# Performance work log

Measured on AMD Instinct MI355X. Metric: run time of the kernel, lower is better.

The kernel has to match this reference:

```python
import jax, jax.numpy as jnp
import numpy as np

D = 256; DFFN = 1024; H = 8; NLVL = 4; NPNT = 4; HD = D // H
BS = 4; NQ = 100; NPTS = 25
SPATIAL = [(128, 128), (64, 64), (32, 32), (16, 16)]
LEN_IN = sum(h * w for h, w in SPATIAL)


def _ln(x, g, b, eps=1e-5):
    m = x.mean(-1, keepdims=True)
    v = ((x - m) ** 2).mean(-1, keepdims=True)
    return (x - m) * jax.lax.rsqrt(v + eps) * g + b


def _mha(q, k, v, w_in, b_in, w_out, b_out):
    # torch nn.MultiheadAttention math, batch-first layout [B,S,D]
    B, Sq, _ = q.shape; Sk = k.shape[1]
    wq, wk, wv = jnp.split(w_in, 3, 0); bq, bk, bv = jnp.split(b_in, 3)
    qh = (q @ wq.T + bq).reshape(B, Sq, H, HD).transpose(0, 2, 1, 3)
    kh = (k @ wk.T + bk).reshape(B, Sk, H, HD).transpose(0, 2, 1, 3)
    vh = (v @ wv.T + bv).reshape(B, Sk, H, HD).transpose(0, 2, 1, 3)
    a = jax.nn.softmax(jnp.einsum('bhqd,bhkd->bhqk', qh, kh) * (1.0 / float(np.sqrt(HD))), -1)
    o = jnp.einsum('bhqk,bhkd->bhqd', a, vh).transpose(0, 2, 1, 3).reshape(B, Sq, D)
    return o @ w_out.T + b_out


def _msdeform(query, ref, src, off_w, off_b, aw_w, aw_b, val_w, val_b, out_w, out_b):
    # MSDeformAttn: per-query multi-level bilinear sampling + weighted aggregation
    bs, Lq, _ = query.shape
    value = (src @ val_w.T + val_b).reshape(bs, LEN_IN, H, HD)
    off = (query @ off_w.T + off_b).reshape(bs, Lq, H, NLVL, NPNT, 2)
    aw = jax.nn.softmax((query @ aw_w.T + aw_b).reshape(bs, Lq, H, NLVL * NPNT), -1)
    aw = aw.reshape(bs, Lq, H, NLVL, NPNT)
    norm = jnp.array([[w, h] for h, w in SPATIAL], jnp.float32)  # (W,H) per level
    loc = ref[:, :, None, :, None, :] + off / norm[None, None, None, :, None, :]
    out = jnp.zeros((bs, H, Lq, HD), query.dtype)
    start = 0
    for l, (hh, ww) in enumerate(SPATIAL):
        v_l = value[:, start:start + hh * ww].transpose(0, 2, 1, 3)  # [bs,H,hw,HD]
        start += hh * ww
        # grid_sample align_corners=False pixel coords: loc*size - 0.5
        x = (loc[:, :, :, l, :, 0] * ww - 0.5).transpose(0, 2, 1, 3).reshape(bs, H, Lq * NPNT)
        y = (loc[:, :, :, l, :, 1] * hh - 0.5).transpose(0, 2, 1, 3).reshape(bs, H, Lq * NPNT)
        x0 = jnp.floor(x); y0 = jnp.floor(y); wx = x - x0; wy = y - y0
        x0i = x0.astype(jnp.int32); y0i = y0.astype(jnp.int32); x1i = x0i + 1; y1i = y0i + 1
        def g(xi, yi):
            valid = ((xi >= 0) & (xi < ww) & (yi >= 0) & (yi < hh)).astype(query.dtype)
            idx = jnp.clip(yi, 0, hh - 1) * ww + jnp.clip(xi, 0, ww - 1)
            return jnp.take_along_axis(v_l, idx[..., None], axis=2) * valid[..., None]
        s = (g(x0i, y0i) * ((1 - wx) * (1 - wy))[..., None]
             + g(x1i, y0i) * (wx * (1 - wy))[..., None]
             + g(x0i, y1i) * ((1 - wx) * wy)[..., None]
             + g(x1i, y1i) * (wx * wy)[..., None])
        s = s.reshape(bs, H, Lq, NPNT, HD)
        out = out + (s * aw[:, :, :, l].transpose(0, 2, 1, 3)[..., None]).sum(3)
    return out.transpose(0, 2, 1, 3).reshape(bs, Lq, D) @ out_w.T + out_b


def _fwd(tgt, query_pos, reference_points, src,
         w_in_intra, b_in_intra, w_out_intra, b_out_intra, g_norm_intra, b_norm_intra,
         w_in_inter, b_in_inter, w_out_inter, b_out_inter, g_norm_inter, b_norm_inter,
         off_w, off_b, aw_w, aw_b, val_w, val_b, co_w, co_b, g_norm_cross, b_norm_cross,
         lin1_w, lin1_b, lin2_w, lin2_b, g_norm3, b_norm3):
    bs, nq, npts, d = tgt.shape
    # intra-instance self-attention (over control points)
    q = (tgt + query_pos).reshape(bs * nq, npts, d)
    t2 = _mha(q, q, tgt.reshape(bs * nq, npts, d), w_in_intra, b_in_intra, w_out_intra, b_out_intra)
    tgt = _ln(tgt + t2.reshape(bs, nq, npts, d), g_norm_intra, b_norm_intra)
    # inter-instance self-attention (over queries), no pos embed per source code
    ti = tgt.transpose(0, 2, 1, 3).reshape(bs * npts, nq, d)
    t2 = _mha(ti, ti, ti, w_in_inter, b_in_inter, w_out_inter, b_out_inter)
    ti = _ln(ti + t2, g_norm_inter, b_norm_inter).reshape(bs, npts, nq, d).transpose(0, 2, 1, 3)
    # deformable cross-attention
    ref = jnp.broadcast_to(reference_points[:, :, None], (bs, nq, npts, NLVL, 2)).reshape(bs, nq * npts, NLVL, 2)
    qc = (ti + query_pos).reshape(bs, nq * npts, d)
    t2 = _msdeform(qc, ref, src, off_w, off_b, aw_w, aw_b, val_w, val_b, co_w, co_b).reshape(bs, nq, npts, d)
    tgt = _ln(ti + t2, g_norm_cross, b_norm_cross)
    # FFN
    ff = jax.nn.relu(tgt @ lin1_w.T + lin1_b) @ lin2_w.T + lin2_b
    return _ln(tgt + ff, g_norm3, b_norm3)


def setup_inputs() -> dict:
    key = jax.random.key(0)
    ki = iter(jax.random.split(key, 40))
    def rn(shape, sc=0.02):
        return jax.random.normal(next(ki), shape, jnp.float32) * sc
    inp = dict(
        tgt=jax.random.normal(next(ki), (BS, NQ, NPTS, D), jnp.float32),
        query_pos=jax.random.normal(next(ki), (BS, NQ, NPTS, D), jnp.float32),
        reference_points=jax.random.uniform(next(ki), (BS, NQ, NLVL, 2), jnp.float32),
        src=jax.random.normal(next(ki), (BS, LEN_IN, D), jnp.float32),
        w_in_intra=rn((3 * D, D)), b_in_intra=jnp.zeros((3 * D,), jnp.float32),
        w_out_intra=rn((D, D)), b_out_intra=jnp.zeros((D,), jnp.float32),
        g_norm_intra=jnp.ones((D,), jnp.float32), b_norm_intra=jnp.zeros((D,), jnp.float32),
        w_in_inter=rn((3 * D, D)), b_in_inter=jnp.zeros((3 * D,), jnp.float32),
        w_out_inter=rn((D, D)), b_out_inter=jnp.zeros((D,), jnp.float32),
        g_norm_inter=jnp.ones((D,), jnp.float32), b_norm_inter=jnp.zeros((D,), jnp.float32),
        off_w=rn((H * NLVL * NPNT * 2, D), 0.001), off_b=rn((H * NLVL * NPNT * 2,), 0.5),
        aw_w=rn((H * NLVL * NPNT, D)), aw_b=jnp.zeros((H * NLVL * NPNT,), jnp.float32),
        val_w=rn((D, D)), val_b=jnp.zeros((D,), jnp.float32),
        co_w=rn((D, D)), co_b=jnp.zeros((D,), jnp.float32),
        g_norm_cross=jnp.ones((D,), jnp.float32), b_norm_cross=jnp.zeros((D,), jnp.float32),
        lin1_w=rn((DFFN, D)), lin1_b=jnp.zeros((DFFN,), jnp.float32),
        lin2_w=rn((D, DFFN)), lin2_b=jnp.zeros((D,), jnp.float32),
        g_norm3=jnp.ones((D,), jnp.float32), b_norm3=jnp.zeros((D,), jnp.float32),
        src_spatial_shapes=jnp.array(SPATIAL, jnp.int32),
        level_start_index=jnp.array(np.cumsum([0] + [h * w for h, w in SPATIAL[:-1]]), jnp.int32),
    )
    return inp


def reference(tgt, query_pos, reference_points, src,
              w_in_intra, b_in_intra, w_out_intra, b_out_intra, g_norm_intra, b_norm_intra,
              w_in_inter, b_in_inter, w_out_inter, b_out_inter, g_norm_inter, b_norm_inter,
              off_w, off_b, aw_w, aw_b, val_w, val_b, co_w, co_b, g_norm_cross, b_norm_cross,
              lin1_w, lin1_b, lin2_w, lin2_b, g_norm3, b_norm3,
              src_spatial_shapes, level_start_index):
    # spatial shapes / level starts are compile-time constants (SPATIAL); args kept for signature parity
    return _fwd(tgt, query_pos, reference_points, src,
                w_in_intra, b_in_intra, w_out_intra, b_out_intra, g_norm_intra, b_norm_intra,
                w_in_inter, b_in_inter, w_out_inter, b_out_inter, g_norm_inter, b_norm_inter,
                off_w, off_b, aw_w, aw_b, val_w, val_b, co_w, co_b, g_norm_cross, b_norm_cross,
                lin1_w, lin1_b, lin2_w, lin2_b, g_norm3, b_norm3)
```

## Files before the change

### kernel.cpp

```cpp
#include <hip/hip_runtime.h>
#include <math.h>

#define DMODEL 256
#define HEADS  8
#define HDIM   32
#define BS     4
#define NQ     100
#define NPTS   25
#define LQ     2500
#define M10K   10000
#define LEN_IN 21760
#define MVAL   87040

typedef float f32x4 __attribute__((ext_vector_type(4)));
typedef short s16x8 __attribute__((ext_vector_type(8)));
typedef unsigned short u16;

static __device__ __forceinline__ short f2bf(float f) {
    unsigned u = __builtin_bit_cast(unsigned, f);
    u = (u + 0x7fffu + ((u >> 16) & 1u)) >> 16;
    return (short)u;
}
static __device__ __forceinline__ unsigned pack2(float lo, float hi) {
    return (unsigned)(u16)f2bf(lo) | ((unsigned)(u16)f2bf(hi) << 16);
}
static __device__ __forceinline__ float bf_lo(unsigned u) {
    return __builtin_bit_cast(float, u << 16);
}
static __device__ __forceinline__ float bf_hi(unsigned u) {
    return __builtin_bit_cast(float, u & 0xffff0000u);
}

#define LDSK   40
#define LDSK64 72

__global__ __launch_bounds__(256) void convert_weights_kernel(
    const float* __restrict__ s0, const float* __restrict__ s1,
    const float* __restrict__ s2, const float* __restrict__ s3,
    const float* __restrict__ s4, const float* __restrict__ s5,
    const float* __restrict__ s6, const float* __restrict__ s7,
    const float* __restrict__ s8, const float* __restrict__ s9,
    u16* __restrict__ dst)
{
    int t8 = (blockIdx.x * 256 + threadIdx.x) * 8;
    if (t8 >= 1277952) return;
    const float* s; int base;
    if      (t8 <  196608) { s = s0; base = 0;       }
    else if (t8 <  262144) { s = s1; base = 196608;  }
    else if (t8 <  458752) { s = s2; base = 262144;  }
    else if (t8 <  524288) { s = s3; base = 458752;  }
    else if (t8 <  589824) { s = s4; base = 524288;  }
    else if (t8 <  622592) { s = s5; base = 589824;  }
    else if (t8 <  688128) { s = s6; base = 622592;  }
    else if (t8 <  753664) { s = s7; base = 688128;  }
    else if (t8 < 1015808) { s = s8; base = 753664;  }
    else                   { s = s9; base = 1015808; }
    const float* p = s + (t8 - base);
    float4 a = *(const float4*)p;
    float4 b = *(const float4*)(p + 4);
    s16x8 v;
    v[0]=f2bf(a.x); v[1]=f2bf(a.y); v[2]=f2bf(a.z); v[3]=f2bf(a.w);
    v[4]=f2bf(b.x); v[5]=f2bf(b.y); v[6]=f2bf(b.z); v[7]=f2bf(b.w);
    *(s16x8*)(dst + t8) = v;
}

__global__ __launch_bounds__(256) void add_convert_kernel(
    const float* __restrict__ a, const float* __restrict__ b,
    u16* __restrict__ xb, u16* __restrict__ ab, int n8)
{
    int i = blockIdx.x * 256 + threadIdx.x;
    if (i >= n8) return;
    size_t o = (size_t)i * 8;
    float4 a0 = *(const float4*)(a + o);
    float4 a1 = *(const float4*)(a + o + 4);
    if (ab) {
        s16x8 v;
        v[0]=f2bf(a0.x); v[1]=f2bf(a0.y); v[2]=f2bf(a0.z); v[3]=f2bf(a0.w);
        v[4]=f2bf(a1.x); v[5]=f2bf(a1.y); v[6]=f2bf(a1.z); v[7]=f2bf(a1.w);
        *(s16x8*)(ab + o) = v;
    }
    if (b) {
        float4 b0 = *(const float4*)(b + o);
        float4 b1 = *(const float4*)(b + o + 4);
        a0.x += b0.x; a0.y += b0.y; a0.z += b0.z; a0.w += b0.w;
        a1.x += b1.x; a1.y += b1.y; a1.z += b1.z; a1.w += b1.w;
    }
    s16x8 v;
    v[0]=f2bf(a0.x); v[1]=f2bf(a0.y); v[2]=f2bf(a0.z); v[3]=f2bf(a0.w);
    v[4]=f2bf(a1.x); v[5]=f2bf(a1.y); v[6]=f2bf(a1.z); v[7]=f2bf(a1.w);
    *(s16x8*)(xb + o) = v;
}

__global__ __launch_bounds__(256) void gemm_mfma_kernel(
    const u16* __restrict__ A, int lda,
    const u16* __restrict__ W, int K,
    const float* __restrict__ bias,
    void* __restrict__ Cv, int ldc,
    int M, int relu, int out_bf16)
{
    __shared__ short As[64 * LDSK64];
    __shared__ short Ws[64 * LDSK64];

    const int tid = threadIdx.x;
    const int m0 = blockIdx.y * 64, n0 = blockIdx.x * 64;
    const int srow = tid >> 2;
    const int sk = (tid & 3) * 16;
    const int wave = tid >> 6;
    const int wm = wave & 1, wn = wave >> 1;
    const int lane = tid & 63;
    const int lrow = lane & 15;
    const int kq = lane >> 4;

    const int gm = m0 + srow;
    const u16* aptr = A + (size_t)gm * lda + sk;
    const u16* wptr = W + (size_t)(n0 + srow) * K + sk;

    f32x4 acc[2][2];
#pragma unroll
    for (int i = 0; i < 2; ++i)
#pragma unroll
        for (int j = 0; j < 2; ++j) acc[i][j] = (f32x4)(0.f);

    s16x8 a0 = (s16x8)0, a1 = (s16x8)0, w0, w1;
    if (gm < M) { a0 = *(const s16x8*)aptr; a1 = *(const s16x8*)(aptr + 8); }
    w0 = *(const s16x8*)wptr; w1 = *(const s16x8*)(wptr + 8);

    for (int k0 = 0; k0 < K; k0 += 64) {
        *(s16x8*)&As[srow * LDSK64 + sk]     = a0;
        *(s16x8*)&As[srow * LDSK64 + sk + 8] = a1;
        *(s16x8*)&Ws[srow * LDSK64 + sk]     = w0;
        *(s16x8*)&Ws[srow * LDSK64 + sk + 8] = w1;
        __syncthreads();
        if (k0 + 64 < K) {
            if (gm < M) {
                a0 = *(const s16x8*)(aptr + k0 + 64);
                a1 = *(const s16x8*)(aptr + k0 + 72);
            }
            w0 = *(const s16x8*)(wptr + k0 + 64);
            w1 = *(const s16x8*)(wptr + k0 + 72);
        }

#pragma unroll
        for (int s = 0; s < 2; ++s) {
            s16x8 af[2], bfv[2];
#pragma unroll
            for (int i = 0; i < 2; ++i)
                af[i] = *(const s16x8*)&As[(wm * 32 + i * 16 + lrow) * LDSK64 + s * 32 + kq * 8];
#pragma unroll
            for (int j = 0; j < 2; ++j)
                bfv[j] = *(const s16x8*)&Ws[(wn * 32 + j * 16 + lrow) * LDSK64 + s * 32 + kq * 8];
#pragma unroll
            for (int i = 0; i < 2; ++i)
#pragma unroll
                for (int j = 0; j < 2; ++j)
                    acc[i][j] = __builtin_amdgcn_mfma_f32_16x16x32_bf16(af[i], bfv[j], acc[i][j], 0, 0, 0);
        }
        __syncthreads();
    }

#pragma unroll
    for (int i = 0; i < 2; ++i)
#pragma unroll
        for (int j = 0; j < 2; ++j) {
            int col = n0 + wn * 32 + j * 16 + lrow;
            float bv = bias[col];
#pragma unroll
            for (int reg = 0; reg < 4; ++reg) {
                int gmo = m0 + wm * 32 + i * 16 + kq * 4 + reg;
                if (gmo < M) {
                    float v = acc[i][j][reg] + bv;
                    if (relu) v = fmaxf(v, 0.f);
                    if (out_bf16)
                        ((u16*)Cv)[(size_t)gmo * ldc + col] = (u16)f2bf(v);
                    else
                        ((float*)Cv)[(size_t)gmo * ldc + col] = v;
                }
            }
        }
}

__global__ __launch_bounds__(256) void gemm_mfma128_kernel(
    const u16* __restrict__ A, int lda,
    const u16* __restrict__ W, int K,
    const float* __restrict__ bias,
    void* __restrict__ Cv, int ldc,
    int M, int relu, int out_bf16)
{
    __shared__ short As[128 * LDSK];
    __shared__ short Ws[128 * LDSK];

    const int tid = threadIdx.x;
    const int m0 = blockIdx.y * 128, n0 = blockIdx.x * 128;

    const int srow = tid >> 1;
    const int sk = (tid & 1) * 16;

    const int wave = tid >> 6;
    const int wm = wave & 1, wn = wave >> 1;
    const int lane = tid & 63;
    const int lrow = lane & 15;
    const int kq = lane >> 4;

    const int gm = m0 + srow;
    const u16* aptr = A + (size_t)gm * lda + sk;
    const u16* wptr = W + (size_t)(n0 + srow) * K + sk;

    f32x4 acc[4][4];
#pragma unroll
    for (int i = 0; i < 4; ++i)
#pragma unroll
        for (int j = 0; j < 4; ++j) acc[i][j] = (f32x4)(0.f);

    s16x8 a0 = (s16x8)0, a1 = (s16x8)0, w0, w1;
    if (gm < M) { a0 = *(const s16x8*)aptr; a1 = *(const s16x8*)(aptr + 8); }
    w0 = *(const s16x8*)wptr; w1 = *(const s16x8*)(wptr + 8);

    for (int k0 = 0; k0 < K; k0 += 32) {
        *(s16x8*)&As[srow * LDSK + sk]     = a0;
        *(s16x8*)&As[srow * LDSK + sk + 8] = a1;
        *(s16x8*)&Ws[srow * LDSK + sk]     = w0;
        *(s16x8*)&Ws[srow * LDSK + sk + 8] = w1;
        __syncthreads();
        if (k0 + 32 < K) {
            if (gm < M) {
                a0 = *(const s16x8*)(aptr + k0 + 32);
                a1 = *(const s16x8*)(aptr + k0 + 40);
            }
            w0 = *(const s16x8*)(wptr + k0 + 32);
            w1 = *(const s16x8*)(wptr + k0 + 40);
        }

        s16x8 af[4], bfv[4];
#pragma unroll
        for (int i = 0; i < 4; ++i)
            af[i] = *(const s16x8*)&As[(wm * 64 + i * 16 + lrow) * LDSK + kq * 8];
#pragma unroll
        for (int j = 0; j < 4; ++j)
            bfv[j] = *(const s16x8*)&Ws[(wn * 64 + j * 16 + lrow) * LDSK + kq * 8];
#pragma unroll
        for (int i = 0; i < 4; ++i)
#pragma unroll
            for (int j = 0; j < 4; ++j)
                acc[i][j] = __builtin_amdgcn_mfma_f32_16x16x32_bf16(af[i], bfv[j], acc[i][j], 0, 0, 0);
        __syncthreads();
    }

#pragma unroll
    for (int i = 0; i < 4; ++i)
#pragma unroll
        for (int j = 0; j < 4; ++j) {
            int col = n0 + wn * 64 + j * 16 + lrow;
            float bv = bias[col];
#pragma unroll
            for (int reg = 0; reg < 4; ++reg) {
                int gmo = m0 + wm * 64 + i * 16 + kq * 4 + reg;
                if (gmo < M) {
                    float v = acc[i][j][reg] + bv;
                    if (relu) v = fmaxf(v, 0.f);
                    if (out_bf16)
                        ((u16*)Cv)[(size_t)gmo * ldc + col] = (u16)f2bf(v);
                    else
                        ((float*)Cv)[(size_t)gmo * ldc + col] = v;
                }
            }
        }
}

__global__ __launch_bounds__(256) void gemm_value64_kernel(
    const float* __restrict__ A,
    const u16* __restrict__ W,
    const float* __restrict__ bias,
    u16* __restrict__ C)
{
    __shared__ short As[64 * LDSK];
    __shared__ short Ws[128 * LDSK];

    const int tid = threadIdx.x;
    const int n0 = blockIdx.x * 128;
    const int m0 = blockIdx.y * 64;

    const int arow = tid >> 2;
    const int ak = (tid & 3) * 8;
    const int wrow = tid >> 1;
    const int wk = (tid & 1) * 16;

    const float* aptr = A + (size_t)(m0 + arow) * 256 + ak;
    const u16* wptr = W + (size_t)(n0 + wrow) * 256 + wk;

    const int wave = tid >> 6;
    const int wm = wave & 1, wn = wave >> 1;
    const int lane = tid & 63;
    const int lrow = lane & 15, kq = lane >> 4;

    f32x4 acc[2][4];
#pragma unroll
    for (int i = 0; i < 2; ++i)
#pragma unroll
        for (int j = 0; j < 4; ++j) acc[i][j] = (f32x4)(0.f);

    float4 pa0 = *(const float4*)aptr;
    float4 pa1 = *(const float4*)(aptr + 4);
    s16x8 w0 = *(const s16x8*)wptr;
    s16x8 w1 = *(const s16x8*)(wptr + 8);

    for (int k0 = 0; k0 < 256; k0 += 32) {
        s16x8 av;
        av[0]=f2bf(pa0.x); av[1]=f2bf(pa0.y); av[2]=f2bf(pa0.z); av[3]=f2bf(pa0.w);
        av[4]=f2bf(pa1.x); av[5]=f2bf(pa1.y); av[6]=f2bf(pa1.z); av[7]=f2bf(pa1.w);
        *(s16x8*)&As[arow * LDSK + ak]     = av;
        *(s16x8*)&Ws[wrow * LDSK + wk]     = w0;
        *(s16x8*)&Ws[wrow * LDSK + wk + 8] = w1;
        __syncthreads();
        if (k0 + 32 < 256) {
            pa0 = *(const float4*)(aptr + k0 + 32);
            pa1 = *(const float4*)(aptr + k0 + 36);
            w0 = *(const s16x8*)(wptr + k0 + 32);
            w1 = *(const s16x8*)(wptr + k0 + 40);
        }

        s16x8 af[2], bfv[4];
#pragma unroll
        for (int i = 0; i < 2; ++i)
            af[i] = *(const s16x8*)&As[(wm * 32 + i * 16 + lrow) * LDSK + kq * 8];
#pragma unroll
        for (int j = 0; j < 4; ++j)
            bfv[j] = *(const s16x8*)&Ws[(wn * 64 + j * 16 + lrow) * LDSK + kq * 8];
#pragma unroll
        for (int i = 0; i < 2; ++i)
#pragma unroll
            for (int j = 0; j < 4; ++j)
                acc[i][j] = __builtin_amdgcn_mfma_f32_16x16x32_bf16(af[i], bfv[j], acc[i][j], 0, 0, 0);
        __syncthreads();
    }

#pragma unroll
    for (int i = 0; i < 2; ++i)
#pragma unroll
        for (int j = 0; j < 4; ++j) {
            int col = n0 + wn * 64 + j * 16 + lrow;
            float bv = bias[col];
#pragma unroll
            for (int reg = 0; reg < 4; ++reg) {
                int gmo = m0 + wm * 32 + i * 16 + kq * 4 + reg;
                C[(size_t)gmo * 256 + col] = (u16)f2bf(acc[i][j][reg] + bv);
            }
        }
}

__global__ __launch_bounds__(256) void inter_attn_mfma_kernel(
    const u16* __restrict__ qkv, u16* __restrict__ out, float scale)
{
    __shared__ __align__(16) u16 Qs[112 * 40];
    __shared__ __align__(16) u16 Ks[112 * 40];
    __shared__ __align__(16) u16 Vt[32 * 136];
    __shared__ __align__(16) u16 Ps[112 * 136];

    const int b = blockIdx.x, h = blockIdx.y;
    const u16* base = qkv + (size_t)b * 100 * 768;
    const int tid = threadIdx.x;
    const int wave = tid >> 6, lane = tid & 63;
    const int lr = lane & 15, quad = lane >> 4;

    for (int i = tid; i < 12 * 20; i += 256) {
        int row = 100 + i / 20, c = (i % 20) * 2;
        *(unsigned*)&Qs[row * 40 + c] = 0;
        *(unsigned*)&Ks[row * 40 + c] = 0;
    }
    for (int i = tid; i < 2176; i += 256) ((unsigned*)Vt)[i] = 0;
    for (int i = tid; i < 7616; i += 256) ((unsigned*)Ps)[i] = 0;
    __syncthreads();

    for (int idx = tid; idx < 2400; idx += 256) {
        int row = idx / 24, s = idx % 24;
        const u16* p = (s < 8)  ? base + row * 768 + h * 32 + s * 4
                     : (s < 16) ? base + row * 768 + 256 + h * 32 + (s - 8) * 4
                                : base + row * 768 + 512 + h * 32 + (s - 16) * 4;
        if (s < 8) {
            *(uint2*)&Qs[row * 40 + s * 4] = *(const uint2*)p;
        } else if (s < 16) {
            *(uint2*)&Ks[row * 40 + (s - 8) * 4] = *(const uint2*)p;
        } else {
            int d0 = (s - 16) * 4;
            Vt[(d0 + 0) * 136 + row] = p[0];
            Vt[(d0 + 1) * 136 + row] = p[1];
            Vt[(d0 + 2) * 136 + row] = p[2];
            Vt[(d0 + 3) * 136 + row] = p[3];
        }
    }
    __syncthreads();

#pragma unroll 1
    for (int rr = 0; rr < 2; ++rr) {
        int rt = wave + rr * 4;
        if (rt < 7) {
            s16x8 aq = *(const s16x8*)&Qs[(rt * 16 + lr) * 40 + quad * 8];
            f32x4 sc[7];
#pragma unroll
            for (int ct = 0; ct < 7; ++ct) {
                s16x8 bk = *(const s16x8*)&Ks[(ct * 16 + lr) * 40 + quad * 8];
                sc[ct] = __builtin_amdgcn_mfma_f32_16x16x32_bf16(aq, bk, (f32x4)(0.f), 0, 0, 0);
            }
            const bool colok[7] = {true, true, true, true, true, true, (lr < 4)};
#pragma unroll
            for (int reg = 0; reg < 4; ++reg) {
                float mx = -1e30f;
#pragma unroll
                for (int ct = 0; ct < 7; ++ct) {
                    float sv = sc[ct][reg] * scale;
                    sc[ct][reg] = sv;
                    if (colok[ct]) mx = fmaxf(mx, sv);
                }
#pragma unroll
                for (int d = 1; d < 16; d <<= 1) mx = fmaxf(mx, __shfl_xor(mx, d));
                float ssum = 0.f;
#pragma unroll
                for (int ct = 0; ct < 7; ++ct) {
                    float pv = colok[ct] ? __expf(sc[ct][reg] - mx) : 0.f;
                    sc[ct][reg] = pv;
                    ssum += pv;
                }
#pragma unroll
                for (int d = 1; d < 16; d <<= 1) ssum += __shfl_xor(ssum, d);
                float inv = 1.f / ssum;
                int prow = rt * 16 + quad * 4 + reg;
#pragma unroll
                for (int ct = 0; ct < 7; ++ct)
                    Ps[prow * 136 + ct * 16 + lr] = (u16)f2bf(sc[ct][reg] * inv);
            }
        }
    }
    __syncthreads();

#pragma unroll 1
    for (int rr = 0; rr < 2; ++rr) {
        int rt = wave + rr * 4;
        if (rt < 7) {
            f32x4 o0 = (f32x4)(0.f), o1 = (f32x4)(0.f);
#pragma unroll
            for (int kk = 0; kk < 4; ++kk) {
                s16x8 ap = *(const s16x8*)&Ps[(rt * 16 + lr) * 136 + kk * 32 + quad * 8];
                s16x8 bv0 = *(const s16x8*)&Vt[lr * 136 + kk * 32 + quad * 8];
                s16x8 bv1 = *(const s16x8*)&Vt[(16 + lr) * 136 + kk * 32 + quad * 8];
                o0 = __builtin_amdgcn_mfma_f32_16x16x32_bf16(ap, bv0, o0, 0, 0, 0);
                o1 = __builtin_amdgcn_mfma_f32_16x16x32_bf16(ap, bv1, o1, 0, 0, 0);
            }
#pragma unroll
            for (int reg = 0; reg < 4; ++reg) {
                int q = rt * 16 + quad * 4 + reg;
                if (q < 100) {
                    u16* op = out + ((size_t)b * 100 + q) * 256 + h * 32;
                    op[lr]      = (u16)f2bf(o0[reg]);
                    op[16 + lr] = (u16)f2bf(o1[reg]);
                }
            }
        }
    }
}

__global__ __launch_bounds__(256) void intra_attn_kernel(
    const float* __restrict__ qkv, u16* __restrict__ out, float scale)
{
    __shared__ float4 KV[25][128];

    const int b = blockIdx.x;
    const int h = threadIdx.x >> 5, r = threadIdx.x & 31;
    const float* base = qkv + (size_t)b * 25 * 768;

    for (int idx = threadIdx.x; idx < 3200; idx += 256) {
        int row = idx >> 7, c = idx & 127;
        KV[row][c] = *(const float4*)(base + row * 768 + 256 + c * 4);
    }

    float q[32];
    if (r < 25) {
        const float* qp = base + r * 768 + h * 32;
#pragma unroll
        for (int c4 = 0; c4 < 8; ++c4) {
            float4 f = *(const float4*)(qp + c4 * 4);
            q[c4*4+0] = f.x; q[c4*4+1] = f.y; q[c4*4+2] = f.z; q[c4*4+3] = f.w;
        }
    }
    __syncthreads();

    if (r < 25) {
        float m = -1e30f, l = 0.f, acc[32];
#pragma unroll
        for (int c = 0; c < 32; ++c) acc[c] = 0.f;
#pragma unroll 2
        for (int j = 0; j < 25; ++j) {
            const float4* kr = &KV[j][h * 8];
            float dot = 0.f;
#pragma unroll
            for (int c4 = 0; c4 < 8; ++c4) {
                float4 kf = kr[c4];
                dot = fmaf(q[c4*4+0], kf.x, dot);
                dot = fmaf(q[c4*4+1], kf.y, dot);
                dot = fmaf(q[c4*4+2], kf.z, dot);
                dot = fmaf(q[c4*4+3], kf.w, dot);
            }
            dot *= scale;
            float mn = fmaxf(m, dot);
            float alpha = __expf(m - mn);
            float p = __expf(dot - mn);
            l = l * alpha + p;
            const float4* vr = &KV[j][64 + h * 8];
#pragma unroll
            for (int c4 = 0; c4 < 8; ++c4) {
                float4 vf = vr[c4];
                acc[c4*4+0] = acc[c4*4+0] * alpha + p * vf.x;
                acc[c4*4+1] = acc[c4*4+1] * alpha + p * vf.y;
                acc[c4*4+2] = acc[c4*4+2] * alpha + p * vf.z;
                acc[c4*4+3] = acc[c4*4+3] * alpha + p * vf.w;
            }
            m = mn;
        }
        float inv = 1.f / l;
        unsigned* op = (unsigned*)(out + ((size_t)b * 25 + r) * 256 + h * 32);
#pragma unroll
        for (int c = 0; c < 16; ++c)
            op[c] = pack2(acc[2*c] * inv, acc[2*c+1] * inv);
    }
}

__global__ __launch_bounds__(64) void add_ln_kernel(
    const float* __restrict__ a, const float* __restrict__ b,
    const float* __restrict__ g, const float* __restrict__ beta,
    float* __restrict__ out, u16* __restrict__ out_bf, int transpose_mode)
{
    const int r = blockIdx.x;
    const int lane = threadIdx.x;
    const float* ar = a + (size_t)r * 256;
    const float* br = b + (size_t)r * 256;
    float x[4];
    float s = 0.f;
#pragma unroll
    for (int i = 0; i < 4; ++i) {
        x[i] = ar[lane + 64 * i] + br[lane + 64 * i];
        s += x[i];
    }
#pragma unroll
    for (int off = 32; off >= 1; off >>= 1) s += __shfl_xor(s, off);
    float mean = s * (1.f / 256.f);
    float vs = 0.f;
#pragma unroll
    for (int i = 0; i < 4; ++i) { float d = x[i] - mean; vs += d * d; }
#pragma unroll
    for (int off = 32; off >= 1; off >>= 1) vs += __shfl_xor(vs, off);
    float rstd = rsqrtf(vs * (1.f / 256.f) + 1e-5f);

    size_t ro = r;
    if (transpose_mode == 1) {
        int q = r % 100; int bp = r / 100; int p = bp % 25; int bb = bp / 25;
        ro = ((size_t)bb * 100 + q) * 25 + p;
    } else if (transpose_mode == 2) {
        int p = r % 25; int t = r / 25; int q = t % 100; int bb = t / 100;
        ro = ((size_t)bb * 25 + p) * 100 + q;
    }
    float* orow = out + ro * 256;
    u16* brow = out_bf ? out_bf + ro * 256 : (u16*)0;
#pragma unroll
    for (int i = 0; i < 4; ++i) {
        int c = lane + 64 * i;
        float v = (x[i] - mean) * rstd * g[c] + beta[c];
        orow[c] = v;
        if (brow) brow[c] = (u16)f2bf(v);
    }
}

__global__ __launch_bounds__(256, 4) void msdeform_sample_kernel(
    const u16* __restrict__ value,
    const float* __restrict__ off,
    const float* __restrict__ awl,
    const float* __restrict__ refp,
    u16* __restrict__ sampled)
{
    const int unit = blockIdx.x * 8 + (threadIdx.x >> 5);
    const int t = threadIdx.x & 31;
    const int h = t >> 2, c8 = t & 3;
    const int b = unit / LQ, lq = unit - b * LQ;
    const int q = lq / NPTS;

    const float* awp = awl + (size_t)unit * 128 + h * 16;
    float w[16];
    float mx = -1e30f;
#pragma unroll
    for (int k = 0; k < 16; ++k) { w[k] = awp[k]; mx = fmaxf(mx, w[k]); }
    float sum = 0.f;
#pragma unroll
    for (int k = 0; k < 16; ++k) { w[k] = __expf(w[k] - mx); sum += w[k]; }
    const float inv = 1.f / sum;

    const float* offp = off + (size_t)unit * 256 + h * 32;
    const float* rp = refp + ((size_t)b * 100 + q) * 8;
    const u16* vbase = value + (size_t)b * LEN_IN * 256 + h * 32 + c8 * 8;

    float acc[8];
#pragma unroll
    for (int k = 0; k < 8; ++k) acc[k] = 0.f;

    int start = 0;
    const int sz[4] = {128, 64, 32, 16};
#pragma unroll
    for (int l = 0; l < 4; ++l) {
        const int hh = sz[l], ww = sz[l];
        const float rx = rp[l * 2 + 0], ry = rp[l * 2 + 1];
#pragma unroll 1
        for (int pt = 0; pt < 4; ++pt) {
            float ox = offp[(l * 4 + pt) * 2 + 0];
            float oy = offp[(l * 4 + pt) * 2 + 1];
            float x = rx * ww + ox - 0.5f;
            float y = ry * hh + oy - 0.5f;
            float x0f = floorf(x), y0f = floorf(y);
            float wx = x - x0f, wy = y - y0f;
            int x0 = (int)x0f, y0 = (int)y0f;
            int x1 = x0 + 1, y1 = y0 + 1;
            float aw = w[l * 4 + pt] * inv;

            int x0c = min(max(x0, 0), ww - 1), x1c = min(max(x1, 0), ww - 1);
            int y0c = min(max(y0, 0), hh - 1), y1c = min(max(y1, 0), hh - 1);
            float w00 = aw * (1.f - wx) * (1.f - wy);
            float w10 = aw * wx * (1.f - wy);
            float w01 = aw * (1.f - wx) * wy;
            float w11 = aw * wx * wy;
            if (!(x0 >= 0 && x0 < ww)) { w00 = 0.f; w01 = 0.f; }
            if (!(x1 >= 0 && x1 < ww)) { w10 = 0.f; w11 = 0.f; }
            if (!(y0 >= 0 && y0 < hh)) { w00 = 0.f; w10 = 0.f; }
            if (!(y1 >= 0 && y1 < hh)) { w01 = 0.f; w11 = 0.f; }

            uint4 u00 = *(const uint4*)(vbase + (size_t)(start + y0c * ww + x0c) * 256);
            uint4 u10 = *(const uint4*)(vbase + (size_t)(start + y0c * ww + x1c) * 256);
            uint4 u01 = *(const uint4*)(vbase + (size_t)(start + y1c * ww + x0c) * 256);
            uint4 u11 = *(const uint4*)(vbase + (size_t)(start + y1c * ww + x1c) * 256);

#define ACC4(u, wgt) \
            acc[0] = fmaf(wgt, bf_lo(u.x), acc[0]); \
            acc[1] = fmaf(wgt, bf_hi(u.x), acc[1]); \
            acc[2] = fmaf(wgt, bf_lo(u.y), acc[2]); \
            acc[3] = fmaf(wgt, bf_hi(u.y), acc[3]); \
            acc[4] = fmaf(wgt, bf_lo(u.z), acc[4]); \
            acc[5] = fmaf(wgt, bf_hi(u.z), acc[5]); \
            acc[6] = fmaf(wgt, bf_lo(u.w), acc[6]); \
            acc[7] = fmaf(wgt, bf_hi(u.w), acc[7]);
            ACC4(u00, w00); ACC4(u10, w10); ACC4(u01, w01); ACC4(u11, w11);
#undef ACC4
        }
        start += hh * ww;
    }

    uint4 pk;
    pk.x = pack2(acc[0], acc[1]); pk.y = pack2(acc[2], acc[3]);
    pk.z = pack2(acc[4], acc[5]); pk.w = pack2(acc[6], acc[7]);
    *(uint4*)(sampled + (size_t)unit * 256 + h * 32 + c8 * 8) = pk;
}

extern "C" void kernel_launch(void* const* d_in, const int* in_sizes, int n_in,
                              void* d_out, int out_size, void* d_ws, size_t ws_size,
                              hipStream_t stream)
{
    (void)in_sizes; (void)n_in; (void)out_size; (void)ws_size;

    const float* tgt        = (const float*)d_in[0];
    const float* query_pos  = (const float*)d_in[1];
    const float* refp       = (const float*)d_in[2];
    const float* src        = (const float*)d_in[3];
    const float* w_in_intra = (const float*)d_in[4];
    const float* b_in_intra = (const float*)d_in[5];
    const float* w_out_intra= (const float*)d_in[6];
    const float* b_out_intra= (const float*)d_in[7];
    const float* g_ln_intra = (const float*)d_in[8];
    const float* b_ln_intra = (const float*)d_in[9];
    const float* w_in_inter = (const float*)d_in[10];
    const float* b_in_inter = (const float*)d_in[11];
    const float* w_out_inter= (const float*)d_in[12];
    const float* b_out_inter= (const float*)d_in[13];
    const float* g_ln_inter = (const float*)d_in[14];
    const float* b_ln_inter = (const float*)d_in[15];
    const float* off_w      = (const float*)d_in[16];
    const float* off_b      = (const float*)d_in[17];
    const float* aw_w       = (const float*)d_in[18];
    const float* aw_b       = (const float*)d_in[19];
    const float* val_w      = (const float*)d_in[20];
    const float* val_b      = (const float*)d_in[21];
    const float* co_w       = (const float*)d_in[22];
    const float* co_b       = (const float*)d_in[23];
    const float* g_ln_cross = (const float*)d_in[24];
    const float* b_ln_cross = (const float*)d_in[25];
    const float* lin1_w     = (const float*)d_in[26];
    const float* lin1_b     = (const float*)d_in[27];
    const float* lin2_w     = (const float*)d_in[28];
    const float* lin2_b     = (const float*)d_in[29];
    const float* g_ln3      = (const float*)d_in[30];
    const float* b_ln3      = (const float*)d_in[31];

    float* ws    = (float*)d_ws;
    float* qkv   = ws;
    float* tmp   = ws + 7680000;
    u16*   attnb = (u16*)(ws + 10240000);
    float* tgt1  = ws + 11520000;
    float* ti    = ws + 14080000;
    u16*   tib   = (u16*)(ws + 16640000);
    float* tA    = ws + 17920000;
    u16*   qcb   = (u16*)(ws + 20480000);
    u16*   x1b   = (u16*)(ws + 21760000);
    u16*   tgtb  = (u16*)(ws + 23040000);
    float* awl   = ws + 24320000;
    u16*   valueb= (u16*)(ws + 25600000);
    u16*   wb    = (u16*)(ws + 36741120);
    float* out   = (float*)d_out;

    u16* qkvb = (u16*)qkv;

    u16* wb_in_intra  = wb;
    u16* wb_out_intra = wb + 196608;
    u16* wb_in_inter  = wb + 262144;
    u16* wb_out_inter = wb + 458752;
    u16* wb_off       = wb + 524288;
    u16* wb_aw        = wb + 589824;
    u16* wb_val       = wb + 622592;
    u16* wb_co        = wb + 688128;
    u16* wb_lin1      = wb + 753664;
    u16* wb_lin2      = wb + 1015808;

    const float scale = 0.17677669529663687f;
    const int MB64  = (M10K + 63) / 64;
    const int MB128 = (M10K + 127) / 128;

    convert_weights_kernel<<<624, 256, 0, stream>>>(
        w_in_intra, w_out_intra, w_in_inter, w_out_inter, off_w,
        aw_w, val_w, co_w, lin1_w, lin2_w, wb);
    add_convert_kernel<<<1250, 256, 0, stream>>>(tgt, query_pos, x1b, tgtb, 320000);

    gemm_mfma128_kernel<<<dim3(4, MB128), 256, 0, stream>>>(x1b, 256, wb_in_intra, 256,
                                                            b_in_intra, qkv, 768, M10K, 0, 0);
    gemm_mfma_kernel<<<dim3(4, MB64), 256, 0, stream>>>(tgtb, 256, wb_in_intra + 512 * 256, 256,
                                                        b_in_intra + 512, qkv + 512, 768, M10K, 0, 0);
    intra_attn_kernel<<<400, 256, 0, stream>>>(qkv, attnb, scale);
    gemm_mfma_kernel<<<dim3(4, MB64), 256, 0, stream>>>(attnb, 256, wb_out_intra, 256,
                                                        b_out_intra, tmp, 256, M10K, 0, 0);
    add_ln_kernel<<<M10K, 64, 0, stream>>>(tgt, tmp, g_ln_intra, b_ln_intra, ti, tib, 2);

    gemm_mfma128_kernel<<<dim3(6, MB128), 256, 0, stream>>>(tib, 256, wb_in_inter, 256,
                                                            b_in_inter, qkvb, 768, M10K, 0, 1);
    inter_attn_mfma_kernel<<<dim3(100, 8), 256, 0, stream>>>(qkvb, attnb, scale);
    gemm_mfma_kernel<<<dim3(4, MB64), 256, 0, stream>>>(attnb, 256, wb_out_inter, 256,
                                                        b_out_inter, tmp, 256, M10K, 0, 0);
    add_ln_kernel<<<M10K, 64, 0, stream>>>(ti, tmp, g_ln_inter, b_ln_inter, tA, (u16*)0, 1);

    add_convert_kernel<<<1250, 256, 0, stream>>>(tA, query_pos, qcb, (u16*)0, 320000);
    gemm_value64_kernel<<<dim3(2, 1360), 256, 0, stream>>>(src, wb_val, val_b, valueb);
    gemm_mfma_kernel<<<dim3(4, MB64), 256, 0, stream>>>(qcb, 256, wb_off, 256,
                                                        off_b, tgt1, 256, M10K, 0, 0);
    gemm_mfma_kernel<<<dim3(2, MB64), 256, 0, stream>>>(qcb, 256, wb_aw, 256,
                                                        aw_b, awl, 128, M10K, 0, 0);
    msdeform_sample_kernel<<<1250, 256, 0, stream>>>(valueb, tgt1, awl, refp, attnb);
    gemm_mfma_kernel<<<dim3(4, MB64), 256, 0, stream>>>(attnb, 256, wb_co, 256,
                                                        co_b, tmp, 256, M10K, 0, 0);
    add_ln_kernel<<<M10K, 64, 0, stream>>>(tA, tmp, g_ln_cross, b_ln_cross, ti, tib, 0);

    gemm_mfma128_kernel<<<dim3(8, MB128), 256, 0, stream>>>(tib, 256, wb_lin1, 256,
                                                            lin1_b, valueb, 1024, M10K, 1, 1);
    gemm_mfma_kernel<<<dim3(4, MB64), 256, 0, stream>>>(valueb, 1024, wb_lin2, 1024,
                                                        lin2_b, tmp, 256, M10K, 0, 0);
    add_ln_kernel<<<M10K, 64, 0, stream>>>(ti, tmp, g_ln3, b_ln3, out, (u16*)0, 0);
}
```

Baseline: 479.2 us.

## Fuse output GEMMs with residual LayerNorm and merge offset/attn-weight GEMMs

Adds a gemm_ln kernel that computes a full 256-column row tile (16 rows per block), then adds bias and residual and applies LayerNorm in the epilogue, optionally writing a bf16 copy and the query_pos-added bf16 query. This replaces four GEMM+add_ln pairs and one add_convert launch, avoiding the fp32 tmp round trips and extra launches. The offset and attention-weight projections are merged into one launch through a column split in the epilogue. The cost is a small 16-row tile that reloads the full weight slice per block, which gives less weight reuse and lower MFMA efficiency, especially for the K=1024 lin2 GEMM.

```diff
diff --git a/kernel.cpp b/kernel.cpp
--- a/kernel.cpp
+++ b/kernel.cpp
@@ -96,7 +96,9 @@
     const u16* __restrict__ W, int K,
     const float* __restrict__ bias,
     void* __restrict__ Cv, int ldc,
-    int M, int relu, int out_bf16)
+    int M, int relu, int out_bf16,
+    int ncut, const float* __restrict__ bias2,
+    float* __restrict__ Cv2, int ldc2)
 {
     __shared__ short As[64 * LDSK64];
     __shared__ short Ws[64 * LDSK64];
@@ -163,17 +165,21 @@
 #pragma unroll
         for (int j = 0; j < 2; ++j) {
             int col = n0 + wn * 32 + j * 16 + lrow;
-            float bv = bias[col];
+            float bv = (col < ncut) ? bias[col] : bias2[col - ncut];
 #pragma unroll
             for (int reg = 0; reg < 4; ++reg) {
                 int gmo = m0 + wm * 32 + i * 16 + kq * 4 + reg;
                 if (gmo < M) {
                     float v = acc[i][j][reg] + bv;
                     if (relu) v = fmaxf(v, 0.f);
-                    if (out_bf16)
-                        ((u16*)Cv)[(size_t)gmo * ldc + col] = (u16)f2bf(v);
-                    else
-                        ((float*)Cv)[(size_t)gmo * ldc + col] = v;
+                    if (col < ncut) {
+                        if (out_bf16)
+                            ((u16*)Cv)[(size_t)gmo * ldc + col] = (u16)f2bf(v);
+                        else
+                            ((float*)Cv)[(size_t)gmo * ldc + col] = v;
+                    } else {
+                        Cv2[(size_t)gmo * ldc2 + (col - ncut)] = v;
+                    }
                 }
             }
         }
@@ -264,6 +270,132 @@
                 }
             }
         }
+}
+
+__global__ __launch_bounds__(256) void gemm_ln_kernel(
+    const u16* __restrict__ A, int lda,
+    const u16* __restrict__ W, int K,
+    const float* __restrict__ bias,
+    const float* __restrict__ res,
+    const float* __restrict__ g, const float* __restrict__ beta,
+    float* __restrict__ outf, u16* __restrict__ outbf,
+    const float* __restrict__ qp, u16* __restrict__ qout,
+    int tmode)
+{
+    __shared__ short As[16 * LDSK];
+    __shared__ short Ws[256 * LDSK];
+    __shared__ float redS[4][16];
+    __shared__ float redV[4][16];
+
+    const int tid = threadIdx.x;
+    const int m0 = blockIdx.x * 16;
+    const int wave = tid >> 6, lane = tid & 63;
+    const int lrow = lane & 15, kq = lane >> 4;
+
+    const u16* aptr = A + (size_t)(m0 + (tid >> 2)) * lda + (tid & 3) * 8;
+    const u16* wptr = W + (size_t)tid * K;
+
+    f32x4 acc[4];
+#pragma unroll
+    for (int j = 0; j < 4; ++j) acc[j] = (f32x4)(0.f);
+
+    s16x8 a0 = (s16x8)0, w0, w1, w2, w3;
+    if (tid < 64) a0 = *(const s16x8*)aptr;
+    w0 = *(const s16x8*)(wptr);
+    w1 = *(const s16x8*)(wptr + 8);
+    w2 = *(const s16x8*)(wptr + 16);
+    w3 = *(const s16x8*)(wptr + 24);
+
+    for (int k0 = 0; k0 < K; k0 += 32) {
+        if (tid < 64) *(s16x8*)&As[(tid >> 2) * LDSK + (tid & 3) * 8] = a0;
+        *(s16x8*)&Ws[tid * LDSK +  0] = w0;
+        *(s16x8*)&Ws[tid * LDSK +  8] = w1;
+        *(s16x8*)&Ws[tid * LDSK + 16] = w2;
+        *(s16x8*)&Ws[tid * LDSK + 24] = w3;
+        __syncthreads();
+        if (k0 + 32 < K) {
+            if (tid < 64) a0 = *(const s16x8*)(aptr + k0 + 32);
+            w0 = *(const s16x8*)(wptr + k0 + 32);
+            w1 = *(const s16x8*)(wptr + k0 + 40);
+            w2 = *(const s16x8*)(wptr + k0 + 48);
+            w3 = *(const s16x8*)(wptr + k0 + 56);
+        }
+
+        s16x8 af = *(const s16x8*)&As[lrow * LDSK + kq * 8];
+#pragma unroll
+        for (int j = 0; j < 4; ++j) {
+            s16x8 bfv = *(const s16x8*)&Ws[(wave * 64 + j * 16 + lrow) * LDSK + kq * 8];
+            acc[j] = __builtin_amdgcn_mfma_f32_16x16x32_bf16(af, bfv, acc[j], 0, 0, 0);
+        }
+        __syncthreads();
+    }
+
+    float x[4][4];
+#pragma unroll
+    for (int j = 0; j < 4; ++j) {
+        const int cj = wave * 64 + j * 16 + lrow;
+        const float bj = bias[cj];
+#pragma unroll
+        for (int reg = 0; reg < 4; ++reg) {
+            const int row = kq * 4 + reg;
+            x[j][reg] = res[(size_t)(m0 + row) * 256 + cj] + acc[j][reg] + bj;
+        }
+    }
+
+#pragma unroll
+    for (int reg = 0; reg < 4; ++reg) {
+        float s = x[0][reg] + x[1][reg] + x[2][reg] + x[3][reg];
+        s += __shfl_xor(s, 1); s += __shfl_xor(s, 2);
+        s += __shfl_xor(s, 4); s += __shfl_xor(s, 8);
+        if (lrow == 0) redS[wave][kq * 4 + reg] = s;
+    }
+    __syncthreads();
+    float mean[4];
+#pragma unroll
+    for (int reg = 0; reg < 4; ++reg) {
+        const int row = kq * 4 + reg;
+        mean[reg] = (redS[0][row] + redS[1][row] + redS[2][row] + redS[3][row]) * (1.f / 256.f);
+    }
+#pragma unroll
+    for (int reg = 0; reg < 4; ++reg) {
+        float vs = 0.f;
+#pragma unroll
+        for (int j = 0; j < 4; ++j) { float d = x[j][reg] - mean[reg]; vs += d * d; }
+        vs += __shfl_xor(vs, 1); vs += __shfl_xor(vs, 2);
+        vs += __shfl_xor(vs, 4); vs += __shfl_xor(vs, 8);
+        if (lrow == 0) redV[wave][kq * 4 + reg] = vs;
+    }
+    __syncthreads();
+    float rstd[4];
+    size_t ro[4];
+#pragma unroll
+    for (int reg = 0; reg < 4; ++reg) {
+        const int row = kq * 4 + reg;
+        rstd[reg] = rsqrtf((redV[0][row] + redV[1][row] + redV[2][row] + redV[3][row]) * (1.f / 256.f) + 1e-5f);
+        const int grow = m0 + row;
+        size_t r = grow;
+        if (tmode == 1) {
+            int q = grow % 100; int bp = grow / 100; int p = bp % 25; int bb = bp / 25;
+            r = ((size_t)bb * 100 + q) * 25 + p;
+        } else if (tmode == 2) {
+            int p = grow % 25; int t = grow / 25; int q = t % 100; int bb = t / 100;
+            r = ((size_t)bb * 25 + p) * 100 + q;
+        }
+        ro[reg] = r;
+    }
+
+#pragma unroll
+    for (int j = 0; j < 4; ++j) {
+        const int cj = wave * 64 + j * 16 + lrow;
+        const float gj = g[cj], bj2 = beta[cj];
+#pragma unroll
+        for (int reg = 0; reg < 4; ++reg) {
+            float y = (x[j][reg] - mean[reg]) * rstd[reg] * gj + bj2;
+            outf[ro[reg] * 256 + cj] = y;
+            if (outbf) outbf[ro[reg] * 256 + cj] = (u16)f2bf(y);
+            if (qout)  qout[ro[reg] * 256 + cj] = (u16)f2bf(y + qp[ro[reg] * 256 + cj]);
+        }
+    }
 }
 
 __global__ __launch_bounds__(256) void gemm_value64_kernel(
@@ -519,51 +651,6 @@
 #pragma unroll
         for (int c = 0; c < 16; ++c)
             op[c] = pack2(acc[2*c] * inv, acc[2*c+1] * inv);
-    }
-}
-
-__global__ __launch_bounds__(64) void add_ln_kernel(
-    const float* __restrict__ a, const float* __restrict__ b,
-    const float* __restrict__ g, const float* __restrict__ beta,
-    float* __restrict__ out, u16* __restrict__ out_bf, int transpose_mode)
-{
-    const int r = blockIdx.x;
-    const int lane = threadIdx.x;
-    const float* ar = a + (size_t)r * 256;
-    const float* br = b + (size_t)r * 256;
-    float x[4];
-    float s = 0.f;
-#pragma unroll
-    for (int i = 0; i < 4; ++i) {
-        x[i] = ar[lane + 64 * i] + br[lane + 64 * i];
-        s += x[i];
-    }
-#pragma unroll
-    for (int off = 32; off >= 1; off >>= 1) s += __shfl_xor(s, off);
-    float mean = s * (1.f / 256.f);
-    float vs = 0.f;
-#pragma unroll
-    for (int i = 0; i < 4; ++i) { float d = x[i] - mean; vs += d * d; }
-#pragma unroll
-    for (int off = 32; off >= 1; off >>= 1) vs += __shfl_xor(vs, off);
-    float rstd = rsqrtf(vs * (1.f / 256.f) + 1e-5f);
-
-    size_t ro = r;
-    if (transpose_mode == 1) {
-        int q = r % 100; int bp = r / 100; int p = bp % 25; int bb = bp / 25;
-        ro = ((size_t)bb * 100 + q) * 25 + p;
-    } else if (transpose_mode == 2) {
-        int p = r % 25; int t = r / 25; int q = t % 100; int bb = t / 100;
-        ro = ((size_t)bb * 25 + p) * 100 + q;
-    }
-    float* orow = out + ro * 256;
-    u16* brow = out_bf ? out_bf + ro * 256 : (u16*)0;
-#pragma unroll
-    for (int i = 0; i < 4; ++i) {
-        int c = lane + 64 * i;
-        float v = (x[i] - mean) * rstd * g[c] + beta[c];
-        orow[c] = v;
-        if (brow) brow[c] = (u16)f2bf(v);
     }
 }
 
@@ -707,6 +794,7 @@
     u16*   valueb= (u16*)(ws + 25600000);
     u16*   wb    = (u16*)(ws + 36741120);
     float* out   = (float*)d_out;
+    (void)tmp;
 
     u16* qkvb = (u16*)qkv;
 
@@ -715,7 +803,6 @@
     u16* wb_in_inter  = wb + 262144;
     u16* wb_out_inter = wb + 458752;
     u16* wb_off       = wb + 524288;
-    u16* wb_aw        = wb + 589824;
     u16* wb_val       = wb + 622592;
     u16* wb_co        = wb + 688128;
     u16* wb_lin1      = wb + 753664;
@@ -724,6 +811,7 @@
     const float scale = 0.17677669529663687f;
     const int MB64  = (M10K + 63) / 64;
     const int MB128 = (M10K + 127) / 128;
+    const int MBLN  = M10K / 16;
 
     convert_weights_kernel<<<624, 256, 0, stream>>>(
         w_in_intra, w_out_intra, w_in_inter, w_out_inter, off_w,
@@ -733,33 +821,32 @@
     gemm_mfma128_kernel<<<dim3(4, MB128), 256, 0, stream>>>(x1b, 256, wb_in_intra, 256,
                                                             b_in_intra, qkv, 768, M10K, 0, 0);
     gemm_mfma_kernel<<<dim3(4, MB64), 256, 0, stream>>>(tgtb, 256, wb_in_intra + 512 * 256, 256,
-                                                        b_in_intra + 512, qkv + 512, 768, M10K, 0, 0);
+                                                        b_in_intra + 512, qkv + 512, 768, M10K, 0, 0,
+                                                        1 << 30, b_in_intra, (float*)0, 0);
     intra_attn_kernel<<<400, 256, 0, stream>>>(qkv, attnb, scale);
-    gemm_mfma_kernel<<<dim3(4, MB64), 256, 0, stream>>>(attnb, 256, wb_out_intra, 256,
-                                                        b_out_intra, tmp, 256, M10K, 0, 0);
-    add_ln_kernel<<<M10K, 64, 0, stream>>>(tgt, tmp, g_ln_intra, b_ln_intra, ti, tib, 2);
+    gemm_ln_kernel<<<MBLN, 256, 0, stream>>>(attnb, 256, wb_out_intra, 256,
+                                             b_out_intra, tgt, g_ln_intra, b_ln_intra,
+                                             ti, tib, (const float*)0, (u16*)0, 2);
 
     gemm_mfma128_kernel<<<dim3(6, MB128), 256, 0, stream>>>(tib, 256, wb_in_inter, 256,
                                                             b_in_inter, qkvb, 768, M10K, 0, 1);
     inter_attn_mfma_kernel<<<dim3(100, 8), 256, 0, stream>>>(qkvb, attnb, scale);
-    gemm_mfma_kernel<<<dim3(4, MB64), 256, 0, stream>>>(attnb, 256, wb_out_inter, 256,
-                                                        b_out_inter, tmp, 256, M10K, 0, 0);
-    add_ln_kernel<<<M10K, 64, 0, stream>>>(ti, tmp, g_ln_inter, b_ln_inter, tA, (u16*)0, 1);
-
-    add_convert_kernel<<<1250, 256, 0, stream>>>(tA, query_pos, qcb, (u16*)0, 320000);
+    gemm_ln_kernel<<<MBLN, 256, 0, stream>>>(attnb, 256, wb_out_inter, 256,
+                                             b_out_inter, ti, g_ln_inter, b_ln_inter,
+                                             tA, (u16*)0, query_pos, qcb, 1);
+
     gemm_value64_kernel<<<dim3(2, 1360), 256, 0, stream>>>(src, wb_val, val_b, valueb);
-    gemm_mfma_kernel<<<dim3(4, MB64), 256, 0, stream>>>(qcb, 256, wb_off, 256,
-                                                        off_b, tgt1, 256, M10K, 0, 0);
-    gemm_mfma_kernel<<<dim3(2, MB64), 256, 0, stream>>>(qcb, 256, wb_aw, 256,
-                                                        aw_b, awl, 128, M10K, 0, 0);
+    gemm_mfma_kernel<<<dim3(6, MB64), 256, 0, stream>>>(qcb, 256, wb_off, 256,
+                                                        off_b, tgt1, 256, M10K, 0, 0,
+                                                        256, aw_b, awl, 128);
     msdeform_sample_kernel<<<1250, 256, 0, stream>>>(valueb, tgt1, awl, refp, attnb);
-    gemm_mfma_kernel<<<dim3(4, MB64), 256, 0, stream>>>(attnb, 256, wb_co, 256,
-                                                        co_b, tmp, 256, M10K, 0, 0);
-    add_ln_kernel<<<M10K, 64, 0, stream>>>(tA, tmp, g_ln_cross, b_ln_cross, ti, tib, 0);
+    gemm_ln_kernel<<<MBLN, 256, 0, stream>>>(attnb, 256, wb_co, 256,
+                                             co_b, tA, g_ln_cross, b_ln_cross,
+                                             ti, tib, (const float*)0, (u16*)0, 0);
 
     gemm_mfma128_kernel<<<dim3(8, MB128), 256, 0, stream>>>(tib, 256, wb_lin1, 256,
                                                             lin1_b, valueb, 1024, M10K, 1, 1);
-    gemm_mfma_kernel<<<dim3(4, MB64), 256, 0, stream>>>(valueb, 1024, wb_lin2, 1024,
-                                                        lin2_b, tmp, 256, M10K, 0, 0);
-    add_ln_kernel<<<M10K, 64, 0, stream>>>(ti, tmp, g_ln3, b_ln3, out, (u16*)0, 0);
-}
+    gemm_ln_kernel<<<MBLN, 256, 0, stream>>>(valueb, 1024, wb_lin2, 1024,
+                                             lin2_b, ti, g_ln3, b_ln3,
+                                             out, (u16*)0, (const float*)0, (u16*)0, 0);
+}
```

Measured after the change: 499.0 us. +4.1%, slower.
